# Kernel tuning notes

Hardware: AMD Instinct MI355X
Metric: run time of the kernel (lower is better)

The kernel has to match this reference:

```python
import jax, jax.numpy as jnp
import numpy as np

TOP_K = 2
CAP_FACTOR = 1.25
MIN_CAPACITY = 4


def setup_inputs() -> dict:
    key = jax.random.key(0)
    k1, k2, k3, k4 = jax.random.split(key, 4)
    B, T, C, E = 8, 2048, 1024, 8
    x = jax.random.normal(k1, (B, T, C), dtype=jnp.float32)
    w_g = jax.random.normal(k2, (E, C), dtype=jnp.float32) * 0.02   # router gate (Linear, no bias)
    c_fc = jax.random.normal(k3, (E, C, 4 * C), dtype=jnp.float32) * 0.02
    c_proj = jax.random.normal(k4, (E, 4 * C, C), dtype=jnp.float32) * 0.02
    return {"x": x, "w_g": w_g, "c_fc": c_fc, "c_proj": c_proj}


def reference(x, w_g, c_fc, c_proj):
    B, T, C = x.shape
    E = w_g.shape[0]
    N = B * T
    capacity = max(MIN_CAPACITY, int(CAP_FACTOR * N * TOP_K / E))  # 5120, static

    xf = x.reshape(N, C)
    # ---- Router (eval path: no noise, no aux losses) ----
    logits = xf @ w_g.T                                   # [N, E]
    top_logits, top_idx = jax.lax.top_k(logits, TOP_K)    # [N, k]
    router_probs = jax.nn.softmax(top_logits, axis=-1)    # [N, k]

    # position in expert: cumsum over (k-major, token) flattened order
    oh = jax.nn.one_hot(top_idx, E, dtype=jnp.int32)      # [N, k, E]
    oh_t = oh.transpose(1, 0, 2).reshape(TOP_K * N, E)
    pos = jnp.cumsum(oh_t, axis=0).reshape(TOP_K, N, E).transpose(1, 0, 2)  # [N, k, E]
    rank = jnp.sum((pos - 1) * oh, axis=-1)               # [N, k], 0-based slot in expert buffer
    valid = rank < capacity                               # capacity mask
    probs_masked = router_probs * valid.astype(router_probs.dtype)
    rank_c = jnp.clip(rank, 0, capacity - 1)

    # ---- Dispatch: scatter tokens into [E, capacity, C] buffers ----
    contrib = xf[:, None, :] * valid[..., None].astype(xf.dtype)  # [N, k, C]
    buf = jnp.zeros((E, capacity, C), dtype=xf.dtype).at[top_idx, rank_c].add(contrib)

    # ---- Experts: bmm -> ReLU^2 -> bmm ----
    h = jnp.einsum('ecd,edf->ecf', buf, c_fc)             # [E, cap, 4C]
    h = jnp.square(jax.nn.relu(h))
    expert_out = jnp.einsum('ecf,efd->ecd', h, c_proj)    # [E, cap, C]

    # ---- Combine: gather expert outputs back, weight by router probs ----
    gathered = expert_out[top_idx, rank_c]                # [N, k, C]
    out = jnp.sum(gathered * probs_masked[..., None], axis=1)
    return out.reshape(B, T, C)
```

## Files before the change

kernel.cpp:

```cpp
#include <hip/hip_runtime.h>

#define NE 8
#define CAP 5120
#define NT 16384
#define CD 1024
#define FCD 4096

typedef __attribute__((ext_vector_type(8))) short short8;
typedef __attribute__((ext_vector_type(4))) float f32x4;

__device__ __forceinline__ unsigned short f2bf(float f) {
  unsigned int u = __builtin_bit_cast(unsigned int, f);
  u += 0x7FFFu + ((u >> 16) & 1u);
  return (unsigned short)(u >> 16);
}
__device__ __forceinline__ float bf2f(unsigned short u) {
  unsigned int v = ((unsigned int)u) << 16;
  return __builtin_bit_cast(float, v);
}
__device__ __forceinline__ void g2lds16(const unsigned short* g, unsigned short* l) {
  __builtin_amdgcn_global_load_lds(
      (const __attribute__((address_space(1))) unsigned int*)(unsigned long long)g,
      (__attribute__((address_space(3))) unsigned int*)l,
      16, 0, 0);
}

__global__ __launch_bounds__(256) void fill_i32_k(int* __restrict__ p, int v, int n) {
  int i = blockIdx.x * 256 + threadIdx.x;
  if (i < n) p[i] = v;
}
__global__ __launch_bounds__(256) void fill_zero_f32x4_k(float4* __restrict__ p, size_t n4) {
  size_t i = (size_t)blockIdx.x * 256 + threadIdx.x;
  if (i < n4) p[i] = make_float4(0.f, 0.f, 0.f, 0.f);
}

__global__ __launch_bounds__(256) void transpose_bf16_k(
    const float* __restrict__ in, unsigned short* __restrict__ out, int R, int Cc) {
  __shared__ float tile[64][65];
  const size_t esz = (size_t)R * Cc;
  const float* inp = in + (size_t)blockIdx.z * esz;
  unsigned short* outp = out + (size_t)blockIdx.z * esz;
  const int cbase = blockIdx.x * 64, rbase = blockIdx.y * 64;
  const int t = threadIdx.x;
#pragma unroll
  for (int i = 0; i < 4; ++i) {
    int idx = i * 256 + t;
    int r = idx >> 4, c4 = (idx & 15) * 4;
    const float4 v = *reinterpret_cast<const float4*>(inp + (size_t)(rbase + r) * Cc + cbase + c4);
    tile[r][c4 + 0] = v.x; tile[r][c4 + 1] = v.y; tile[r][c4 + 2] = v.z; tile[r][c4 + 3] = v.w;
  }
  __syncthreads();
#pragma unroll
  for (int i = 0; i < 4; ++i) {
    int idx = i * 256 + t;
    int oc = idx >> 4, q = (idx & 15) * 4;
    ushort4 o;
    o.x = f2bf(tile[q + 0][oc]); o.y = f2bf(tile[q + 1][oc]);
    o.z = f2bf(tile[q + 2][oc]); o.w = f2bf(tile[q + 3][oc]);
    *reinterpret_cast<ushort4*>(outp + (size_t)(cbase + oc) * R + rbase + q) = o;
  }
}

__global__ __launch_bounds__(256) void router_k(
    const float* __restrict__ x, const float* __restrict__ wg,
    unsigned short* __restrict__ xb, int* __restrict__ topidx, float* __restrict__ probs) {
  __shared__ float wls[NE * CD];
  const int t = threadIdx.x;
  {
    const float4* w4 = (const float4*)wg;
    float4* l4 = (float4*)wls;
    for (int i = t; i < NE * CD / 4; i += 256) l4[i] = w4[i];
  }
  __syncthreads();
  const int wave = t >> 6, lane = t & 63;
  const int gw = blockIdx.x * 4 + wave;
  const float4* wls4 = (const float4*)wls;
#pragma unroll
  for (int it = 0; it < 2; ++it) {
    const int n = gw * 2 + it;
    const float4* xr4 = (const float4*)(x + (size_t)n * CD);
    ushort4* xb4 = (ushort4*)(xb + (size_t)n * CD);
    double acc[NE] = {0, 0, 0, 0, 0, 0, 0, 0};
#pragma unroll
    for (int j = 0; j < 4; ++j) {
      const int idx = j * 64 + lane;
      const float4 xv = xr4[idx];
      ushort4 o;
      o.x = f2bf(xv.x); o.y = f2bf(xv.y); o.z = f2bf(xv.z); o.w = f2bf(xv.w);
      xb4[idx] = o;
#pragma unroll
      for (int e = 0; e < NE; ++e) {
        const float4 wv = wls4[e * 256 + idx];
        acc[e] += (double)xv.x * (double)wv.x + (double)xv.y * (double)wv.y
                + (double)xv.z * (double)wv.z + (double)xv.w * (double)wv.w;
      }
    }
#pragma unroll
    for (int s = 32; s >= 1; s >>= 1) {
#pragma unroll
      for (int e = 0; e < NE; ++e) acc[e] += __shfl_xor(acc[e], s, 64);
    }
    if (lane == 0) {
      int i1 = 0; double v1 = acc[0];
      for (int e = 1; e < NE; ++e) if (acc[e] > v1) { v1 = acc[e]; i1 = e; }
      int i2 = -1; double v2 = -1e300;
      for (int e = 0; e < NE; ++e) if (e != i1 && acc[e] > v2) { v2 = acc[e]; i2 = e; }
      float p0 = 1.0f / (1.0f + expf((float)(v2 - v1)));
      topidx[n * 2 + 0] = i1; topidx[n * 2 + 1] = i2;
      probs[n * 2 + 0] = p0; probs[n * 2 + 1] = 1.0f - p0;
    }
  }
}

__global__ __launch_bounds__(256) void hist_k(const int* __restrict__ topidx, int* __restrict__ blkhist) {
  __shared__ int h[16];
  const int t = threadIdx.x;
  if (t < 16) h[t] = 0;
  __syncthreads();
  const int n = blockIdx.x * 256 + t;
  atomicAdd(&h[topidx[n * 2 + 0]], 1);
  atomicAdd(&h[8 + topidx[n * 2 + 1]], 1);
  __syncthreads();
  if (t < 16) blkhist[blockIdx.x * 16 + t] = h[t];
}

__global__ void scan_k(const int* __restrict__ blkhist, int* __restrict__ blkoff, int* __restrict__ totals_cnt) {
  const int t = threadIdx.x;
  if (t < 16) {
    int s = 0;
    for (int b = 0; b < 64; ++b) { blkoff[b * 16 + t] = s; s += blkhist[b * 16 + t]; }
    totals_cnt[t] = s;
  }
  __syncthreads();
  if (t < 8) {
    int tot = totals_cnt[t] + totals_cnt[8 + t];
    totals_cnt[16 + t] = tot < CAP ? tot : CAP;
  }
}

__global__ __launch_bounds__(256) void rank_k(
    const int* __restrict__ topidx, const int* __restrict__ blkoff,
    const int* __restrict__ totals_cnt, int* __restrict__ ranks, int* __restrict__ slotmap) {
  __shared__ int wcnt[2][4][8];
  __shared__ int woff[2][4][8];
  const int t = threadIdx.x, wave = t >> 6, lane = t & 63;
  const int n = blockIdx.x * 256 + t;
  const int e1 = topidx[n * 2 + 0], e2 = topidx[n * 2 + 1];
  const unsigned long long lt = (1ull << lane) - 1ull;
  int pre1 = 0, pre2 = 0;
#pragma unroll
  for (int e = 0; e < 8; ++e) {
    unsigned long long m1 = __ballot(e1 == e);
    unsigned long long m2 = __ballot(e2 == e);
    if (e1 == e) pre1 = __popcll(m1 & lt);
    if (e2 == e) pre2 = __popcll(m2 & lt);
    if (lane == 0) { wcnt[0][wave][e] = __popcll(m1); wcnt[1][wave][e] = __popcll(m2); }
  }
  __syncthreads();
  if (t < 16) {
    int k = t >> 3, e = t & 7, s = 0;
    for (int w = 0; w < 4; ++w) { woff[k][w][e] = s; s += wcnt[k][w][e]; }
  }
  __syncthreads();
  int r1 = blkoff[blockIdx.x * 16 + e1] + woff[0][wave][e1] + pre1;
  int r2 = totals_cnt[e2] + blkoff[blockIdx.x * 16 + 8 + e2] + woff[1][wave][e2] + pre2;
  ranks[n * 2 + 0] = (r1 < CAP) ? r1 : -1;
  ranks[n * 2 + 1] = (r2 < CAP) ? r2 : -1;
  if (r1 < CAP) slotmap[e1 * CAP + r1] = n * 2 + 0;
  if (r2 < CAP) slotmap[e2 * CAP + r2] = n * 2 + 1;
}

template <int BM, int TN>
__device__ __forceinline__ bool map_tile(const int* cnt, int e_base, int n_le,
                                         int& le, int& mt, int& nt) {
  constexpr int TM = CAP / BM;
  int pref[9];
  int L = 0;
  for (int i = 0; i < n_le; ++i) {
    pref[i] = L;
    int lm = (cnt[e_base + i] + BM - 1) / BM;
    if (lm > TM) lm = TM;
    L += lm;
  }
  const int totalLive = L * TN;
  const int bid = blockIdx.x;
  if (bid >= totalLive) return false;
  const int q = totalLive >> 3, r = totalLive & 7;
  const int xcd = bid & 7, lin = bid >> 3;
  const int wid = (xcd < r ? xcd * (q + 1) : r * (q + 1) + (xcd - r) * q) + lin;
  const int pair = wid / TN;
  nt = wid % TN;
  le = n_le - 1;
  for (int i = 1; i < n_le; ++i) if (pair < pref[i]) { le = i - 1; break; }
  mt = pair - pref[le];
  return true;
}

template <int BM, int KDIM, int NDIM, bool GATHER, bool RELU2>
__global__ __launch_bounds__(512) void gemm8p_k(
    const unsigned short* __restrict__ A, const unsigned short* __restrict__ Bt,
    unsigned short* __restrict__ Out, const int* __restrict__ slotmap,
    const int* __restrict__ cnt, int e_base, int n_le) {
  constexpr int BN = 256;
  constexpr int KT = KDIM / 64;
  constexpr int TN = NDIM / BN;
  constexpr int M_REP = BM / 32;
  constexpr int QM = M_REP / 2;
  constexpr int AL = BM / 128;
  constexpr int BL = 2;
  constexpr int V = AL + BL;

  __shared__ unsigned short lA[2][BM * 64];
  __shared__ unsigned short lB[2][BN * 64];

  int le, mt, nt;
  if (!map_tile<BM, TN>(cnt, e_base, n_le, le, mt, nt)) return;
  const int e = e_base + le;

  const int tid = threadIdx.x;
  const int wave = tid >> 6, lane = tid & 63;
  const int wr = wave >> 2, wc = wave & 3;
  const int l15 = lane & 15, l4 = lane >> 4;

  const unsigned short* sApt[2][AL];
  const unsigned short* sBpt[2][BL];
#pragma unroll
  for (int h = 0; h < 2; ++h) {
#pragma unroll
    for (int j = 0; j < AL; ++j) {
      const int lc = j * 512 + tid;
      const int lr = lc >> 3, pc = lc & 7;
      const int logc = pc ^ (lr & 7);
      const int rowT = h * (BM / 2) + lr;
      size_t grow;
      if (GATHER) {
        const int sv = slotmap[e * CAP + mt * BM + rowT];
        grow = (size_t)(sv < 0 ? 0 : (sv >> 1));
      } else {
        grow = (size_t)le * CAP + mt * BM + rowT;
      }
      sApt[h][j] = A + grow * KDIM + logc * 8;
    }
#pragma unroll
    for (int j = 0; j < BL; ++j) {
      const int lc = j * 512 + tid;
      const int lr = lc >> 3, pc = lc & 7;
      const int logc = pc ^ (lr & 7);
      sBpt[h][j] = Bt + ((size_t)le * NDIM + nt * BN + h * 128 + lr) * KDIM + logc * 8;
    }
  }

#define STAGE_A(sl, h, tt)                                                              \
  do { _Pragma("unroll") for (int j = 0; j < AL; ++j)                                   \
    g2lds16(sApt[h][j] + (size_t)(tt) * 64,                                             \
            &lA[sl][((h) * (BM / 2) * 8 + j * 512 + wave * 64) * 8]); } while (0)
#define STAGE_B(sl, h, tt)                                                              \
  do { _Pragma("unroll") for (int j = 0; j < BL; ++j)                                   \
    g2lds16(sBpt[h][j] + (size_t)(tt) * 64,                                             \
            &lB[sl][((h) * 128 * 8 + j * 512 + wave * 64) * 8]); } while (0)

  const int kidx0 = ((0 * 4 + l4) ^ (l15 & 7)) * 8;
  const int kidx1 = ((1 * 4 + l4) ^ (l15 & 7)) * 8;

#define RD_A(mh)                                                                        \
  do { _Pragma("unroll") for (int m = 0; m < QM; ++m) {                                 \
    const int row = (mh) * (BM / 2) + wr * (BM / 4) + m * 16 + l15;                     \
    aF[m][0] = *(const short8*)(bA + row * 64 + kidx0);                                 \
    aF[m][1] = *(const short8*)(bA + row * 64 + kidx1); } } while (0)
#define RD_B(DST, nh)                                                                   \
  do { _Pragma("unroll") for (int n = 0; n < 2; ++n) {                                  \
    const int row = (nh) * 128 + wc * 32 + n * 16 + l15;                                \
    DST[n][0] = *(const short8*)(bB + row * 64 + kidx0);                                \
    DST[n][1] = *(const short8*)(bB + row * 64 + kidx1); } } while (0)
#define LGK0()                                                                          \
  do { asm volatile("s_waitcnt lgkmcnt(0)" ::: "memory");                               \
       __builtin_amdgcn_sched_barrier(0); } while (0)
#define MF(BARR, mh, nh)                                                                \
  do { __builtin_amdgcn_s_setprio(1);                                                   \
    _Pragma("unroll") for (int m = 0; m < QM; ++m)                                      \
      _Pragma("unroll") for (int n = 0; n < 2; ++n) {                                   \
        acc[(mh) * QM + m][(nh) * 2 + n] = __builtin_amdgcn_mfma_f32_16x16x32_bf16(     \
            aF[m][0], BARR[n][0], acc[(mh) * QM + m][(nh) * 2 + n], 0, 0, 0);           \
        acc[(mh) * QM + m][(nh) * 2 + n] = __builtin_amdgcn_mfma_f32_16x16x32_bf16(     \
            aF[m][1], BARR[n][1], acc[(mh) * QM + m][(nh) * 2 + n], 0, 0, 0); }         \
    __builtin_amdgcn_s_setprio(0); } while (0)
#define VMC_V()  do { if constexpr (V == 4) asm volatile("s_waitcnt vmcnt(4)" ::: "memory"); \
                      else asm volatile("s_waitcnt vmcnt(3)" ::: "memory"); } while (0)
#define VMC_2()  asm volatile("s_waitcnt vmcnt(2)" ::: "memory")
#define VMC_0()  asm volatile("s_waitcnt vmcnt(0)" ::: "memory")
#define BAR()    do { __builtin_amdgcn_s_barrier(); asm volatile("" ::: "memory"); } while (0)

  f32x4 acc[M_REP][4] = {};
  short8 aF[QM][2], bF0[2][2], bF1[2][2];

  STAGE_A(0, 0, 0); STAGE_B(0, 0, 0); STAGE_B(0, 1, 0); STAGE_A(0, 1, 0);
  VMC_V();
  BAR();

  int s = 0;
  for (int t = 0; t < KT; ++t) {
    const int s2 = s ^ 1;
    const unsigned short* bA = &lA[s][0];
    const unsigned short* bB = &lB[s][0];
    const bool more = (t + 1 < KT);

    RD_A(0); RD_B(bF0, 0);
    if (more) { STAGE_A(s2, 0, t + 1); VMC_V(); } else { VMC_2(); }
    LGK0();
    MF(bF0, 0, 0);
    BAR();
    RD_B(bF1, 1);
    if (more) { STAGE_B(s2, 0, t + 1); VMC_V(); } else { VMC_0(); }
    LGK0();
    MF(bF1, 0, 1);
    BAR();
    RD_A(1);
    if (more) STAGE_B(s2, 1, t + 1);
    LGK0();
    MF(bF1, 1, 1);
    if (more) { STAGE_A(s2, 1, t + 1); VMC_V(); }
    MF(bF0, 1, 0);
    if (more) BAR();
    s = s2;
  }

  const size_t rowb = (size_t)le * CAP + mt * BM;
  const int colb = nt * BN;
#pragma unroll
  for (int i = 0; i < M_REP; ++i) {
    const int mh = i / QM, m = i % QM;
#pragma unroll
    for (int j = 0; j < 4; ++j) {
      const int nh = j / 2, n = j % 2;
#pragma unroll
      for (int rr = 0; rr < 4; ++rr) {
        float v = acc[i][j][rr];
        if (RELU2) { v = fmaxf(v, 0.0f); v = v * v; }
        const size_t orow = rowb + mh * (BM / 2) + wr * (BM / 4) + m * 16 + l4 * 4 + rr;
        Out[orow * NDIM + colb + nh * 128 + wc * 32 + n * 16 + l15] = f2bf(v);
      }
    }
  }
#undef STAGE_A
#undef STAGE_B
#undef RD_A
#undef RD_B
#undef LGK0
#undef MF
#undef VMC_V
#undef VMC_2
#undef VMC_0
#undef BAR
}

template <int WM, int WN, int BM, int BN, int KDIM, int NDIM, bool GATHER, bool RELU2>
__global__ __launch_bounds__(WM * WN * 64) void gemm8_k(
    const unsigned short* __restrict__ A, const unsigned short* __restrict__ Bt,
    unsigned short* __restrict__ Out, const int* __restrict__ slotmap,
    const int* __restrict__ cnt, int e_base, int n_le) {
  constexpr int THREADS = WM * WN * 64;
  constexpr int KT = KDIM / 32;
  constexpr int TN = NDIM / BN;
  constexpr int M_REP = BM / WM / 16;
  constexpr int N_REP = BN / WN / 16;
  constexpr int MH = M_REP / 2;
  constexpr int ALOADS = BM * 4 / THREADS;
  constexpr int BLOADS = BN * 4 / THREADS;
  static_assert(ALOADS + BLOADS == 4, "vmcnt literal assumes 4 loads/wave/tile");

  __shared__ unsigned short lA[3][BM * 32];
  __shared__ unsigned short lB[3][BN * 32];

  int le, mt, nt;
  if (!map_tile<BM, TN>(cnt, e_base, n_le, le, mt, nt)) return;
  const int e = e_base + le;

  const int tid = threadIdx.x;
  const int wave = tid >> 6, lane = tid & 63;
  const int wr = wave / WN, wc = wave % WN;
  const int l15 = lane & 15, l4 = lane >> 4;

  const unsigned short* pA[ALOADS];
  const unsigned short* pB[BLOADS];
#pragma unroll
  for (int j = 0; j < ALOADS; ++j) {
    const int ci = j * THREADS + tid;
    const int row = ci >> 2, cst = ci & 3;
    const int csrc = cst ^ ((row >> 1) & 3);
    size_t grow;
    if (GATHER) {
      const int sv = slotmap[e * CAP + mt * BM + row];
      grow = (size_t)(sv < 0 ? 0 : (sv >> 1));
    } else {
      grow = (size_t)le * CAP + mt * BM + row;
    }
    pA[j] = A + grow * KDIM + csrc * 8;
  }
#pragma unroll
  for (int j = 0; j < BLOADS; ++j) {
    const int ci = j * THREADS + tid;
    const int row = ci >> 2, cst = ci & 3;
    const int csrc = cst ^ ((row >> 1) & 3);
    pB[j] = Bt + ((size_t)le * NDIM + nt * BN + row) * KDIM + csrc * 8;
  }

  const int ksw = (l4 ^ ((l15 >> 1) & 3)) * 8;
  int aOff[M_REP], bOff[N_REP];
#pragma unroll
  for (int m = 0; m < M_REP; ++m)
    aOff[m] = (wr * (BM / WM) + m * 16 + l15) * 32 + ksw;
#pragma unroll
  for (int n = 0; n < N_REP; ++n)
    bOff[n] = (wc * (BN / WN) + n * 16 + l15) * 32 + ksw;

  f32x4 acc[M_REP][N_REP] = {};

#pragma unroll
  for (int kt = 0; kt < 2; ++kt) {
#pragma unroll
    for (int j = 0; j < ALOADS; ++j)
      g2lds16(pA[j] + kt * 32, &lA[kt][(j * THREADS + wave * 64) * 8]);
#pragma unroll
    for (int j = 0; j < BLOADS; ++j)
      g2lds16(pB[j] + kt * 32, &lB[kt][(j * THREADS + wave * 64) * 8]);
  }

  for (int t = 0; t < KT; ++t) {
    if (t < KT - 1) asm volatile("s_waitcnt vmcnt(4)" ::: "memory");
    else            asm volatile("s_waitcnt vmcnt(0)" ::: "memory");
    __builtin_amdgcn_s_barrier();
    asm volatile("" ::: "memory");

    const int s = t % 3, s2 = (t + 2) % 3;
    const unsigned short* sA = &lA[s][0];
    const unsigned short* sB = &lB[s][0];
    const bool pf = (t + 2 < KT);

    short8 aF[MH], bF[N_REP];
#pragma unroll
    for (int m = 0; m < MH; ++m) aF[m] = *(const short8*)(sA + aOff[m]);
#pragma unroll
    for (int n = 0; n < N_REP; ++n) bF[n] = *(const short8*)(sB + bOff[n]);
    if (pf) {
#pragma unroll
      for (int j = 0; j < ALOADS; ++j)
        g2lds16(pA[j] + (t + 2) * 32, &lA[s2][(j * THREADS + wave * 64) * 8]);
    }
    asm volatile("s_waitcnt lgkmcnt(0)" ::: "memory");
    __builtin_amdgcn_sched_barrier(0);
    __builtin_amdgcn_s_setprio(1);
#pragma unroll
    for (int m = 0; m < MH; ++m)
#pragma unroll
      for (int n = 0; n < N_REP; ++n)
        acc[m][n] = __builtin_amdgcn_mfma_f32_16x16x32_bf16(aF[m], bF[n], acc[m][n], 0, 0, 0);
    __builtin_amdgcn_s_setprio(0);

    short8 aG[MH];
#pragma unroll
    for (int m = 0; m < MH; ++m) aG[m] = *(const short8*)(sA + aOff[MH + m]);
    if (pf) {
#pragma unroll
      for (int j = 0; j < BLOADS; ++j)
        g2lds16(pB[j] + (t + 2) * 32, &lB[s2][(j * THREADS + wave * 64) * 8]);
    }
    asm volatile("s_waitcnt lgkmcnt(0)" ::: "memory");
    __builtin_amdgcn_sched_barrier(0);
    __builtin_amdgcn_s_setprio(1);
#pragma unroll
    for (int m = 0; m < MH; ++m)
#pragma unroll
      for (int n = 0; n < N_REP; ++n)
        acc[MH + m][n] = __builtin_amdgcn_mfma_f32_16x16x32_bf16(aG[m], bF[n], acc[MH + m][n], 0, 0, 0);
    __builtin_amdgcn_s_setprio(0);
  }

  const size_t rowb = (size_t)le * CAP + mt * BM + wr * (BM / WM);
  const int colb = nt * BN + wc * (BN / WN);
#pragma unroll
  for (int m = 0; m < M_REP; ++m)
#pragma unroll
    for (int n = 0; n < N_REP; ++n)
#pragma unroll
      for (int rr = 0; rr < 4; ++rr) {
        float v = acc[m][n][rr];
        if (RELU2) { v = fmaxf(v, 0.0f); v = v * v; }
        Out[(rowb + m * 16 + l4 * 4 + rr) * NDIM + colb + n * 16 + l15] = f2bf(v);
      }
}

__global__ __launch_bounds__(256) void combine_k(
    const unsigned short* __restrict__ eo, const int* __restrict__ topidx,
    const float* __restrict__ probs, const int* __restrict__ ranks, float* __restrict__ out) {
  const int n = blockIdx.x, t = threadIdx.x;
  const int c = t * 4;
  const int e1 = topidx[n * 2 + 0], e2 = topidx[n * 2 + 1];
  const int r1 = ranks[n * 2 + 0], r2 = ranks[n * 2 + 1];
  const float p1 = probs[n * 2 + 0], p2 = probs[n * 2 + 1];
  float o0 = 0.f, o1 = 0.f, o2 = 0.f, o3 = 0.f;
  if (r1 >= 0) {
    const ushort4 v = *(const ushort4*)(eo + ((size_t)e1 * CAP + r1) * CD + c);
    o0 += p1 * bf2f(v.x); o1 += p1 * bf2f(v.y); o2 += p1 * bf2f(v.z); o3 += p1 * bf2f(v.w);
  }
  if (r2 >= 0) {
    const ushort4 v = *(const ushort4*)(eo + ((size_t)e2 * CAP + r2) * CD + c);
    o0 += p2 * bf2f(v.x); o1 += p2 * bf2f(v.y); o2 += p2 * bf2f(v.z); o3 += p2 * bf2f(v.w);
  }
  float4 o; o.x = o0; o.y = o1; o.z = o2; o.w = o3;
  *reinterpret_cast<float4*>(out + (size_t)n * CD + c) = o;
}

extern "C" void kernel_launch(void* const* d_in, const int* in_sizes, int n_in,
                              void* d_out, int out_size, void* d_ws, size_t ws_size,
                              hipStream_t stream) {
  const float* x = (const float*)d_in[0];
  const float* wg = (const float*)d_in[1];
  const float* cfc = (const float*)d_in[2];
  const float* cproj = (const float*)d_in[3];
  float* out = (float*)d_out;
  char* ws = (char*)d_ws;
  (void)in_sizes; (void)n_in; (void)out_size;

  const size_t W1SZ = (size_t)FCD * CD * 2;
  const size_t HSZ  = (size_t)CAP * FCD * 2;
  const size_t EOSZ = (size_t)CAP * CD * 2;

  size_t off = 0;
  auto alloc = [&](size_t bytes) { size_t o = off; off = (off + bytes + 255) & ~(size_t)255; return o; };
  unsigned short* XB = (unsigned short*)(ws + alloc((size_t)NT * CD * 2));
  int* TOPIDX  = (int*)(ws + alloc((size_t)NT * 2 * 4));
  float* PROBS = (float*)(ws + alloc((size_t)NT * 2 * 4));
  int* RANKS   = (int*)(ws + alloc((size_t)NT * 2 * 4));
  int* SLOTMAP = (int*)(ws + alloc((size_t)NE * CAP * 4));
  int* BLKHIST = (int*)(ws + alloc(64 * 16 * 4));
  int* BLKOFF  = (int*)(ws + alloc(64 * 16 * 4));
  int* TOTALS  = (int*)(ws + alloc(256));
  const size_t shared_end = off;
  int* CNT = TOTALS + 16;

  size_t woff = shared_end;
  auto walloc = [&](size_t bytes) { size_t o = woff; woff = (woff + bytes + 255) & ~(size_t)255; return o; };
  const size_t oCFCT   = walloc(NE * W1SZ);
  const size_t oCPROJT = walloc(NE * W1SZ);
  const size_t weights_end = woff;

  int EG = 0;
  for (int g = 8; g >= 1; g >>= 1) {
    size_t need = weights_end + NE * EOSZ + 512 + (size_t)g * HSZ + 512;
    if (ws_size >= need) { EG = g; break; }
  }
  if (EG == 0) {
    fill_zero_f32x4_k<<<(NT * CD / 4 + 255) / 256, 256, 0, stream>>>((float4*)out, (size_t)NT * CD / 4);
    return;
  }

  fill_i32_k<<<(NE * CAP + 255) / 256, 256, 0, stream>>>(SLOTMAP, -1, NE * CAP);
  router_k<<<2048, 256, 0, stream>>>(x, wg, XB, TOPIDX, PROBS);
  hist_k<<<64, 256, 0, stream>>>(TOPIDX, BLKHIST);
  scan_k<<<1, 64, 0, stream>>>(BLKHIST, BLKOFF, TOTALS);
  rank_k<<<64, 256, 0, stream>>>(TOPIDX, BLKOFF, TOTALS, RANKS, SLOTMAP);

  unsigned short* CFCT   = (unsigned short*)(ws + oCFCT);
  unsigned short* CPROJT = (unsigned short*)(ws + oCPROJT);
  transpose_bf16_k<<<dim3(FCD / 64, CD / 64, NE), 256, 0, stream>>>(cfc, CFCT, CD, FCD);
  transpose_bf16_k<<<dim3(CD / 64, FCD / 64, NE), 256, 0, stream>>>(cproj, CPROJT, FCD, CD);

  size_t eoff = weights_end;
  auto ealloc = [&](size_t bytes) { size_t o = eoff; eoff = (eoff + bytes + 255) & ~(size_t)255; return o; };
  unsigned short* EO = (unsigned short*)(ws + ealloc(NE * EOSZ));
  unsigned short* H  = (unsigned short*)(ws + ealloc((size_t)EG * HSZ));

  for (int g = 0; g < NE / EG; ++g) {
    const int eb = g * EG;
    gemm8p_k<256, CD, FCD, true, true>
        <<<EG * (CAP / 256) * (FCD / 256), 512, 0, stream>>>(
        XB, CFCT + (size_t)eb * FCD * CD, H, SLOTMAP, CNT, eb, EG);
    gemm8_k<2, 2, 128, 128, FCD, CD, false, false>
        <<<EG * (CAP / 128) * (CD / 128), 256, 0, stream>>>(
        H, CPROJT + (size_t)eb * CD * FCD, EO + (size_t)eb * CAP * CD, SLOTMAP, CNT, eb, EG);
  }
  combine_k<<<NT, 256, 0, stream>>>(EO, TOPIDX, PROBS, RANKS, out);
}
```

Before: 873.2 us.

## Fuse combine into down-projection GEMM epilogue via atomic scatter-add

The second expert GEMM now scatters its fp32 results directly into the output. Each row is scaled by its router probability and added with atomicAdd through the slot map. This removes the bf16 expert-output buffer, the separate combine kernel and its gather traffic. In exchange the output must be zeroed up front, and the epilogue issues many scalar fp32 atomics, each token receiving two contributions. The summation order also becomes nondeterministic.

```diff
diff --git a/kernel.cpp b/kernel.cpp
--- a/kernel.cpp
+++ b/kernel.cpp
@@ -353,11 +353,12 @@
 #undef BAR
 }
 
-template <int WM, int WN, int BM, int BN, int KDIM, int NDIM, bool GATHER, bool RELU2>
+template <int WM, int WN, int BM, int BN, int KDIM, int NDIM, bool GATHER, bool RELU2, bool SCATTER>
 __global__ __launch_bounds__(WM * WN * 64) void gemm8_k(
     const unsigned short* __restrict__ A, const unsigned short* __restrict__ Bt,
     unsigned short* __restrict__ Out, const int* __restrict__ slotmap,
-    const int* __restrict__ cnt, int e_base, int n_le) {
+    const int* __restrict__ cnt, int e_base, int n_le,
+    const float* __restrict__ probs, float* __restrict__ outp) {
   constexpr int THREADS = WM * WN * 64;
   constexpr int KT = KDIM / 32;
   constexpr int TN = NDIM / BN;
@@ -475,39 +476,36 @@
     __builtin_amdgcn_s_setprio(0);
   }
 
-  const size_t rowb = (size_t)le * CAP + mt * BM + wr * (BM / WM);
-  const int colb = nt * BN + wc * (BN / WN);
-#pragma unroll
-  for (int m = 0; m < M_REP; ++m)
-#pragma unroll
-    for (int n = 0; n < N_REP; ++n)
+  if (SCATTER) {
+    const int colb = nt * BN + wc * (BN / WN);
+#pragma unroll
+    for (int m = 0; m < M_REP; ++m) {
 #pragma unroll
       for (int rr = 0; rr < 4; ++rr) {
-        float v = acc[m][n][rr];
-        if (RELU2) { v = fmaxf(v, 0.0f); v = v * v; }
-        Out[(rowb + m * 16 + l4 * 4 + rr) * NDIM + colb + n * 16 + l15] = f2bf(v);
+        const int rl = mt * BM + wr * (BM / WM) + m * 16 + l4 * 4 + rr;
+        const int sv = slotmap[e * CAP + rl];
+        if (sv < 0) continue;
+        const float p = probs[sv];
+        float* ob = outp + (size_t)(sv >> 1) * CD + colb + l15;
+#pragma unroll
+        for (int n = 0; n < N_REP; ++n)
+          atomicAdd(&ob[n * 16], p * acc[m][n][rr]);
       }
-}
-
-__global__ __launch_bounds__(256) void combine_k(
-    const unsigned short* __restrict__ eo, const int* __restrict__ topidx,
-    const float* __restrict__ probs, const int* __restrict__ ranks, float* __restrict__ out) {
-  const int n = blockIdx.x, t = threadIdx.x;
-  const int c = t * 4;
-  const int e1 = topidx[n * 2 + 0], e2 = topidx[n * 2 + 1];
-  const int r1 = ranks[n * 2 + 0], r2 = ranks[n * 2 + 1];
-  const float p1 = probs[n * 2 + 0], p2 = probs[n * 2 + 1];
-  float o0 = 0.f, o1 = 0.f, o2 = 0.f, o3 = 0.f;
-  if (r1 >= 0) {
-    const ushort4 v = *(const ushort4*)(eo + ((size_t)e1 * CAP + r1) * CD + c);
-    o0 += p1 * bf2f(v.x); o1 += p1 * bf2f(v.y); o2 += p1 * bf2f(v.z); o3 += p1 * bf2f(v.w);
-  }
-  if (r2 >= 0) {
-    const ushort4 v = *(const ushort4*)(eo + ((size_t)e2 * CAP + r2) * CD + c);
-    o0 += p2 * bf2f(v.x); o1 += p2 * bf2f(v.y); o2 += p2 * bf2f(v.z); o3 += p2 * bf2f(v.w);
-  }
-  float4 o; o.x = o0; o.y = o1; o.z = o2; o.w = o3;
-  *reinterpret_cast<float4*>(out + (size_t)n * CD + c) = o;
+    }
+  } else {
+    const size_t rowb = (size_t)le * CAP + mt * BM + wr * (BM / WM);
+    const int colb = nt * BN + wc * (BN / WN);
+#pragma unroll
+    for (int m = 0; m < M_REP; ++m)
+#pragma unroll
+      for (int n = 0; n < N_REP; ++n)
+#pragma unroll
+        for (int rr = 0; rr < 4; ++rr) {
+          float v = acc[m][n][rr];
+          if (RELU2) { v = fmaxf(v, 0.0f); v = v * v; }
+          Out[(rowb + m * 16 + l4 * 4 + rr) * NDIM + colb + n * 16 + l15] = f2bf(v);
+        }
+  }
 }
 
 extern "C" void kernel_launch(void* const* d_in, const int* in_sizes, int n_in,
@@ -523,7 +521,6 @@
 
   const size_t W1SZ = (size_t)FCD * CD * 2;
   const size_t HSZ  = (size_t)CAP * FCD * 2;
-  const size_t EOSZ = (size_t)CAP * CD * 2;
 
   size_t off = 0;
   auto alloc = [&](size_t bytes) { size_t o = off; off = (off + bytes + 255) & ~(size_t)255; return o; };
@@ -546,7 +543,7 @@
 
   int EG = 0;
   for (int g = 8; g >= 1; g >>= 1) {
-    size_t need = weights_end + NE * EOSZ + 512 + (size_t)g * HSZ + 512;
+    size_t need = weights_end + (size_t)g * HSZ + 512;
     if (ws_size >= need) { EG = g; break; }
   }
   if (EG == 0) {
@@ -555,6 +552,7 @@
   }
 
   fill_i32_k<<<(NE * CAP + 255) / 256, 256, 0, stream>>>(SLOTMAP, -1, NE * CAP);
+  fill_zero_f32x4_k<<<(NT * CD / 4 + 255) / 256, 256, 0, stream>>>((float4*)out, (size_t)NT * CD / 4);
   router_k<<<2048, 256, 0, stream>>>(x, wg, XB, TOPIDX, PROBS);
   hist_k<<<64, 256, 0, stream>>>(TOPIDX, BLKHIST);
   scan_k<<<1, 64, 0, stream>>>(BLKHIST, BLKOFF, TOTALS);
@@ -565,19 +563,15 @@
   transpose_bf16_k<<<dim3(FCD / 64, CD / 64, NE), 256, 0, stream>>>(cfc, CFCT, CD, FCD);
   transpose_bf16_k<<<dim3(CD / 64, FCD / 64, NE), 256, 0, stream>>>(cproj, CPROJT, FCD, CD);
 
-  size_t eoff = weights_end;
-  auto ealloc = [&](size_t bytes) { size_t o = eoff; eoff = (eoff + bytes + 255) & ~(size_t)255; return o; };
-  unsigned short* EO = (unsigned short*)(ws + ealloc(NE * EOSZ));
-  unsigned short* H  = (unsigned short*)(ws + ealloc((size_t)EG * HSZ));
+  unsigned short* H = (unsigned short*)(ws + weights_end);
 
   for (int g = 0; g < NE / EG; ++g) {
     const int eb = g * EG;
     gemm8p_k<256, CD, FCD, true, true>
         <<<EG * (CAP / 256) * (FCD / 256), 512, 0, stream>>>(
         XB, CFCT + (size_t)eb * FCD * CD, H, SLOTMAP, CNT, eb, EG);
-    gemm8_k<2, 2, 128, 128, FCD, CD, false, false>
+    gemm8_k<2, 2, 128, 128, FCD, CD, false, false, true>
         <<<EG * (CAP / 128) * (CD / 128), 256, 0, stream>>>(
-        H, CPROJT + (size_t)eb * CD * FCD, EO + (size_t)eb * CAP * CD, SLOTMAP, CNT, eb, EG);
-  }
-  combine_k<<<NT, 256, 0, stream>>>(EO, TOPIDX, PROBS, RANKS, out);
-}
+        H, CPROJT + (size_t)eb * CD * FCD, nullptr, SLOTMAP, CNT, eb, EG, PROBS, out);
+  }
+}
```

Measured after the change: 883.5 us. No clear change (+1.2%).
